# Kernel optimization log

Measured on AMD Instinct MI355X. Metric: run time of the kernel, lower is better.

The kernel has to match this reference:

```python
import jax, jax.numpy as jnp
import numpy as np

L, B, S, D, W = 3, 32, 512, 512, 3
EPS = 1e-6

def setup_inputs() -> dict:
    key = jax.random.key(0)
    ks = jax.random.split(key, 12)
    s = 1.0 / np.sqrt(D)
    def n(k, shape, scale=1.0):
        return jax.random.normal(k, shape, dtype=jnp.float32) * scale
    return {
        'x': n(ks[0], (B, S, D)),
        'fwd_pad': n(ks[1], (L, W, D), s),
        'bwd_pad': n(ks[2], (L, W, D), s),
        'fwd_w': n(ks[3], (L, W + 1)),
        'bwd_w': n(ks[4], (L, W + 1)),
        'fwd_w1': n(ks[5], (L, D, D), s),
        'fwd_b1': jnp.zeros((L, D), jnp.float32),
        'fwd_w2': n(ks[6], (L, D, D), s),
        'fwd_b2': jnp.zeros((L, D), jnp.float32),
        'fwd_g': jnp.ones((L, D), jnp.float32),
        'fwd_beta': jnp.zeros((L, D), jnp.float32),
        'bwd_w1': n(ks[7], (L, D, D), s),
        'bwd_b1': jnp.zeros((L, D), jnp.float32),
        'bwd_w2': n(ks[8], (L, D, D), s),
        'bwd_b2': jnp.zeros((L, D), jnp.float32),
        'bwd_g': jnp.ones((L, D), jnp.float32),
        'bwd_beta': jnp.zeros((L, D), jnp.float32),
    }

def _ln(y, g, b):
    # Annotated-transformer LayerNorm: a2*(x-mean)/(std+eps)+b2, unbiased std
    m = y.mean(-1, keepdims=True)
    sd = jnp.std(y, -1, keepdims=True, ddof=1)
    return g * (y - m) / (sd + EPS) + b

def _ffn(y, w1, b1, w2, b2):
    h = jax.nn.relu(jnp.einsum('bsd,de->bse', y, w1) + b1)
    return jnp.einsum('bse,ef->bsf', h, w2) + b2

def _wsum(padded, w, seq_len, offset):
    # weighted sum over a sliding window of width W+1 (dropout=0, eval mode)
    win = jnp.stack([padded[:, offset + k: offset + k + seq_len] for k in range(W + 1)], 0)
    return jnp.einsum('k,kbsd->bsd', w, win)

def reference(x, fwd_pad, bwd_pad, fwd_w, bwd_w,
              fwd_w1, fwd_b1, fwd_w2, fwd_b2, fwd_g, fwd_beta,
              bwd_w1, bwd_b1, bwd_w2, bwd_b2, bwd_g, bwd_beta):
    bsz, seq_len, _ = x.shape
    xf, xb = x, x
    outs = []
    for i in range(L):
        fp = jnp.broadcast_to(fwd_pad[i], (bsz, W, D))
        bp = jnp.broadcast_to(bwd_pad[i], (bsz, W, D))
        pf = jnp.concatenate([fp, xf, bp], axis=1)  # [B, S+2W, D]
        pb = jnp.concatenate([fp, xb, bp], axis=1)
        yf = _wsum(pf, fwd_w[i], seq_len, 0)       # windows [t, t+W]
        yb = _wsum(pb, bwd_w[i], seq_len, W)       # windows [t+W, t+2W]
        xf = yf + _ffn(_ln(yf, fwd_g[i], fwd_beta[i]), fwd_w1[i], fwd_b1[i], fwd_w2[i], fwd_b2[i])
        xb = yb + _ffn(_ln(yb, bwd_g[i], bwd_beta[i]), bwd_w1[i], bwd_b1[i], bwd_w2[i], bwd_b2[i])
        outs.append(jnp.concatenate([xf, xb], axis=-1))
    return jnp.stack(outs, 0)  # [L, B, S, 2D]
```

## Files before the change

kernel.cpp:

```cpp
#include <hip/hip_runtime.h>

#define S_LEN 512
#define D_DIM 512
#define BATCH 32
#define M_ROWS (BATCH * S_LEN)
#define NLAYER 3

typedef unsigned short ushort_t;
typedef __bf16 bf16_t;
typedef bf16_t bf16x8 __attribute__((ext_vector_type(8)));
typedef unsigned short u16x8 __attribute__((ext_vector_type(8)));
typedef float f32x4 __attribute__((ext_vector_type(4)));

typedef const __attribute__((address_space(1))) unsigned int* gptr_t;
typedef __attribute__((address_space(3))) unsigned int* lptr_t;

__device__ __forceinline__ ushort_t f2bf(float f) {
  unsigned u = __float_as_uint(f);
  unsigned r = (u + 0x7fffu + ((u >> 16) & 1u)) >> 16;
  return (ushort_t)r;
}

__device__ __forceinline__ float4 f4fma(float w, float4 u, float4 a) {
  a.x = fmaf(w, u.x, a.x); a.y = fmaf(w, u.y, a.y);
  a.z = fmaf(w, u.z, a.z); a.w = fmaf(w, u.w, a.w);
  return a;
}

__global__ __launch_bounds__(256)
void wprep_kernel(const float* __restrict__ fw1, const float* __restrict__ fw2,
                  const float* __restrict__ bw1, const float* __restrict__ bw2,
                  ushort_t* __restrict__ wt1, ushort_t* __restrict__ wt2) {
  int z = blockIdx.z;
  int l = z >> 2, m = z & 3;
  const float* bases[4] = {fw1, fw2, bw1, bw2};
  const float* src = bases[m] + (size_t)l * D_DIM * D_DIM;
  int streamIdx = m >> 1;
  int which = m & 1;
  ushort_t* dst = (which ? wt2 : wt1) + ((size_t)streamIdx * NLAYER + l) * D_DIM * D_DIM;

  __shared__ float tile[32][33];
  int n0 = blockIdx.x * 32, k0 = blockIdx.y * 32;
  int tx = threadIdx.x, ty = threadIdx.y;
#pragma unroll
  for (int i = 0; i < 32; i += 8)
    tile[ty + i][tx] = src[(size_t)(k0 + ty + i) * D_DIM + n0 + tx];
  __syncthreads();
#pragma unroll
  for (int i = 0; i < 32; i += 8)
    dst[(size_t)(n0 + ty + i) * D_DIM + k0 + tx] = f2bf(tile[tx][ty + i]);
}

__global__ __launch_bounds__(256, 4)
void conv_ln_kernel(const float* __restrict__ srcF, int strideF,
                    const float* __restrict__ srcB, int strideB,
                    const float* __restrict__ padLo, const float* __restrict__ padHi,
                    const float* __restrict__ wF, const float* __restrict__ wB,
                    const float* __restrict__ gF, const float* __restrict__ beF,
                    const float* __restrict__ gB, const float* __restrict__ beB,
                    ushort_t* __restrict__ yln) {
  int z = blockIdx.y;
  int tid = threadIdx.x;
  int lane = tid & 63;
  int wid = tid >> 6;
  int row0 = (blockIdx.x * 4 + wid) * 4;
  int t0 = row0 & (S_LEN - 1);
  const float* src = z ? srcB : srcF;
  int stride = z ? strideB : strideF;
  const float* wv = z ? wB : wF;
  const float* gv = z ? gB : gF;
  const float* bv = z ? beB : beF;
  int toff = z ? 0 : -3;
  int c0 = lane * 4, c1 = 256 + lane * 4;

  float w0 = wv[0], w1 = wv[1], w2 = wv[2], w3 = wv[3];

  float4 u0[7], u1[7];
#pragma unroll
  for (int q = 0; q < 7; ++q) {
    int tt = t0 + toff + q;
    const float* rp;
    if (tt < 0)            rp = padLo + (size_t)(tt + 3) * D_DIM;
    else if (tt >= S_LEN)  rp = padHi + (size_t)(tt - S_LEN) * D_DIM;
    else                   rp = src + (size_t)(row0 + toff + q) * stride;
    u0[q] = *(const float4*)(rp + c0);
    u1[q] = *(const float4*)(rp + c1);
  }

  float4 g0 = *(const float4*)(gv + c0), g1 = *(const float4*)(gv + c1);
  float4 b0 = *(const float4*)(bv + c0), b1 = *(const float4*)(bv + c1);

  float4 y0[4], y1[4];
#pragma unroll
  for (int j = 0; j < 4; ++j) {
    float4 a = make_float4(0.f, 0.f, 0.f, 0.f);
    a = f4fma(w0, u0[j], a); a = f4fma(w1, u0[j + 1], a);
    a = f4fma(w2, u0[j + 2], a); a = f4fma(w3, u0[j + 3], a);
    y0[j] = a;
    float4 c = make_float4(0.f, 0.f, 0.f, 0.f);
    c = f4fma(w0, u1[j], c); c = f4fma(w1, u1[j + 1], c);
    c = f4fma(w2, u1[j + 2], c); c = f4fma(w3, u1[j + 3], c);
    y1[j] = c;
  }

  float s[4], s2[4];
#pragma unroll
  for (int j = 0; j < 4; ++j) {
    float4 a = y0[j], c = y1[j];
    s[j] = a.x + a.y + a.z + a.w + c.x + c.y + c.z + c.w;
    float t = a.x * a.x;
    t = fmaf(a.y, a.y, t); t = fmaf(a.z, a.z, t); t = fmaf(a.w, a.w, t);
    t = fmaf(c.x, c.x, t); t = fmaf(c.y, c.y, t); t = fmaf(c.z, c.z, t);
    t = fmaf(c.w, c.w, t);
    s2[j] = t;
  }

#pragma unroll
  for (int o = 32; o; o >>= 1) {
#pragma unroll
    for (int j = 0; j < 4; ++j) {
      s[j]  += __shfl_xor(s[j],  o);
      s2[j] += __shfl_xor(s2[j], o);
    }
  }

  size_t base = ((size_t)z * M_ROWS + row0) * D_DIM;
#pragma unroll
  for (int j = 0; j < 4; ++j) {
    float mean = s[j] * (1.0f / 512.0f);
    float qv = fmaf(-512.0f * mean, mean, s2[j]);
    qv = fmaxf(qv, 0.0f);
    float sd = sqrtf(qv * (1.0f / 511.0f));
    float inv = 1.0f / (sd + 1e-6f);
    ushort_t p0[4], p1[4];
    p0[0] = f2bf(g0.x * ((y0[j].x - mean) * inv) + b0.x);
    p0[1] = f2bf(g0.y * ((y0[j].y - mean) * inv) + b0.y);
    p0[2] = f2bf(g0.z * ((y0[j].z - mean) * inv) + b0.z);
    p0[3] = f2bf(g0.w * ((y0[j].w - mean) * inv) + b0.w);
    p1[0] = f2bf(g1.x * ((y1[j].x - mean) * inv) + b1.x);
    p1[1] = f2bf(g1.y * ((y1[j].y - mean) * inv) + b1.y);
    p1[2] = f2bf(g1.z * ((y1[j].z - mean) * inv) + b1.z);
    p1[3] = f2bf(g1.w * ((y1[j].w - mean) * inv) + b1.w);
    *(uint2*)(yln + base + (size_t)j * D_DIM + c0) = *(uint2*)p0;
    *(uint2*)(yln + base + (size_t)j * D_DIM + c1) = *(uint2*)p1;
  }
}

#define PHASE_PRE()                                         \
  __builtin_amdgcn_sched_barrier(0);                        \
  __builtin_amdgcn_s_barrier();                             \
  asm volatile("s_waitcnt lgkmcnt(0)" ::: "memory");        \
  __builtin_amdgcn_sched_barrier(0);                        \
  __builtin_amdgcn_s_setprio(1);

#define PHASE_PRE_NOLGKM()                                  \
  __builtin_amdgcn_sched_barrier(0);                        \
  __builtin_amdgcn_s_barrier();                             \
  __builtin_amdgcn_s_setprio(1);

#define PHASE_POST()                                        \
  __builtin_amdgcn_s_setprio(0);                            \
  __builtin_amdgcn_sched_barrier(0);                        \
  __builtin_amdgcn_s_barrier();

#define GROUP_END_CK4()                                     \
  __builtin_amdgcn_s_setprio(0);                            \
  __builtin_amdgcn_sched_barrier(0);                        \
  asm volatile("s_waitcnt vmcnt(4)" ::: "memory");          \
  __builtin_amdgcn_sched_barrier(0);                        \
  __builtin_amdgcn_s_barrier();

#define GROUP_END_CK0()                                     \
  __builtin_amdgcn_s_setprio(0);                            \
  __builtin_amdgcn_sched_barrier(0);                        \
  asm volatile("s_waitcnt vmcnt(0)" ::: "memory");          \
  __builtin_amdgcn_sched_barrier(0);                        \
  __builtin_amdgcn_s_barrier();

#define READ_A(MH)                                                        \
  _Pragma("unroll")                                                       \
  for (int m_ = 0; m_ < 4; ++m_) {                                        \
    _Pragma("unroll")                                                     \
    for (int kk_ = 0; kk_ < 2; ++kk_) {                                   \
      int row_ = ((MH) * 4 + m_) * 32 + wr16lm;                           \
      int idx_ = (row_ * 64 + kk_ * 32 + lq * 8) ^ ((row_ & 7) * 8);      \
      union { u16x8 u; bf16x8 b; } t_;                                    \
      t_.u = *(const u16x8*)&pa[idx_];                                    \
      aF[kk_][m_] = t_.b;                                                 \
    }                                                                     \
  }

#define READ_B(NH)                                                        \
  _Pragma("unroll")                                                       \
  for (int n_ = 0; n_ < 2; ++n_) {                                        \
    _Pragma("unroll")                                                     \
    for (int kk_ = 0; kk_ < 2; ++kk_) {                                   \
      int row_ = ((NH) * 2 + n_) * 64 + wc16lm;                           \
      int idx_ = (row_ * 64 + kk_ * 32 + lq * 8) ^ ((row_ & 7) * 8);      \
      union { u16x8 u; bf16x8 b; } t_;                                    \
      t_.u = *(const u16x8*)&pb[idx_];                                    \
      bF[NH][kk_][n_] = t_.b;                                             \
    }                                                                     \
  }

#define MFMA16(MH, NH)                                                    \
  _Pragma("unroll")                                                       \
  for (int kk_ = 0; kk_ < 2; ++kk_)                                       \
    _Pragma("unroll")                                                     \
    for (int m_ = 0; m_ < 4; ++m_)                                        \
      _Pragma("unroll")                                                   \
      for (int n_ = 0; n_ < 2; ++n_)                                      \
        acc[(MH) * 4 + m_][(NH) * 2 + n_] =                               \
            __builtin_amdgcn_mfma_f32_16x16x32_bf16(                      \
                aF[kk_][m_], bF[NH][kk_][n_],                             \
                acc[(MH) * 4 + m_][(NH) * 2 + n_], 0, 0, 0);

template <int EPI>
__global__ __launch_bounds__(512, 2)
void gemm256_kernel(const ushort_t* __restrict__ A,
                    const ushort_t* __restrict__ Bt_f, const ushort_t* __restrict__ Bt_b,
                    const float* __restrict__ bias_f, const float* __restrict__ bias_b,
                    ushort_t* __restrict__ Hout,
                    float* __restrict__ Cout,
                    const float* __restrict__ srcF, const float* __restrict__ srcB,
                    int srcStride,
                    const float* __restrict__ padLo, const float* __restrict__ padHi,
                    const float* __restrict__ wF, const float* __restrict__ wB) {
  const int K = 512;
  int bid = blockIdx.x;
  int G = (bid & 7) * 32 + (bid >> 3);
  int z = G >> 7;
  int t2 = G & 127;
  int mblk = t2 >> 1, nblk = t2 & 1;
  int row0 = mblk * 256, n0 = nblk * 256;

  const ushort_t* Ab = A + (size_t)z * M_ROWS * K + (size_t)row0 * K;
  const ushort_t* Bb = (z ? Bt_b : Bt_f) + (size_t)n0 * K;

  __shared__ __attribute__((aligned(16))) ushort_t As[2][256 * 64];
  __shared__ __attribute__((aligned(16))) ushort_t Bs[2][256 * 64];

  int tid = threadIdx.x, lane = tid & 63, wave = tid >> 6;
  int wr = wave >> 2, wc = wave & 3;
  int lm = lane & 15, lq = lane >> 4;
  int wr16lm = wr * 16 + lm;
  int wc16lm = wc * 16 + lm;

  auto STAGE = [&](const ushort_t* src, ushort_t* dstBase, int half, int g) {
#pragma unroll
    for (int u = 0; u < 2; ++u) {
      int ch = u * 512 + tid;
      int r = ch >> 3;
      int cs = ((ch & 7) ^ (r & 7)) * 8;
      __builtin_amdgcn_global_load_lds(
          (gptr_t)(const void*)(src + (size_t)(half * 128 + r) * 512 + g * 64 + cs),
          (lptr_t)(void*)(dstBase + (half * 128 + r) * 64 + (ch & 7) * 8), 16, 0, 0);
    }
  };

  f32x4 acc[8][4] = {};
  bf16x8 aF[2][4];
  bf16x8 bF[2][2][2];

  STAGE(Ab, &As[0][0], 0, 0);
  STAGE(Bb, &Bs[0][0], 0, 0);
  STAGE(Ab, &As[0][0], 1, 0);
  STAGE(Bb, &Bs[0][0], 1, 0);
  STAGE(Ab, &As[1][0], 0, 1);
  STAGE(Bb, &Bs[1][0], 0, 1);
  asm volatile("s_waitcnt vmcnt(4)" ::: "memory");
  __builtin_amdgcn_sched_barrier(0);
  __builtin_amdgcn_s_barrier();

#pragma unroll
  for (int g = 0; g < 8; ++g) {
    const ushort_t* pa = &As[g & 1][0];
    const ushort_t* pb = &Bs[g & 1][0];
    ushort_t* oa = &As[(g & 1) ^ 1][0];
    ushort_t* ob = &Bs[(g & 1) ^ 1][0];
    ushort_t* ca = &As[g & 1][0];
    ushort_t* cb = &Bs[g & 1][0];

    READ_A(0)
    READ_B(0)
    if (g + 1 < 8) STAGE(Ab, oa, 1, g + 1);
    PHASE_PRE()
    MFMA16(0, 0)
    PHASE_POST()

    READ_B(1)
    if (g + 1 < 8) STAGE(Bb, ob, 1, g + 1);
    PHASE_PRE()
    MFMA16(0, 1)
    PHASE_POST()

    READ_A(1)
    if (g + 2 < 8) STAGE(Ab, ca, 0, g + 2);
    PHASE_PRE()
    MFMA16(1, 0)
    PHASE_POST()

    if (g + 2 < 8) STAGE(Bb, cb, 0, g + 2);
    PHASE_PRE_NOLGKM()
    MFMA16(1, 1)
    if (g < 6) {
      GROUP_END_CK4()
    } else if (g == 6) {
      GROUP_END_CK0()
    } else {
      PHASE_POST()
    }
  }

  const float* bias = z ? bias_b : bias_f;
  if (EPI == 1) {
    ushort_t* Hb = Hout + (size_t)z * M_ROWS * 512;
#pragma unroll
    for (int mf = 0; mf < 8; ++mf) {
      int mbase = row0 + (mf * 2 + wr) * 16 + lq * 4;
#pragma unroll
      for (int nf = 0; nf < 4; ++nf) {
        int n = n0 + (nf * 4 + wc) * 16 + lm;
        float bvn = bias[n];
#pragma unroll
        for (int r = 0; r < 4; ++r) {
          float v = fmaxf(acc[mf][nf][r] + bvn, 0.0f);
          Hb[(size_t)(mbase + r) * 512 + n] = f2bf(v);
        }
      }
    }
  } else {
    const float* src = z ? srcB : srcF;
    const float* wv = z ? wB : wF;
    int toff = z ? 0 : -3;
    float w0 = wv[0], w1 = wv[1], w2 = wv[2], w3 = wv[3];
    float* Cb = Cout + (size_t)z * 512;
#pragma unroll
    for (int mf = 0; mf < 8; ++mf) {
      int mbase = row0 + (mf * 2 + wr) * 16 + lq * 4;
      int t0 = mbase & (S_LEN - 1);
      int rb = mbase - t0;
      const float* rp[7];
#pragma unroll
      for (int q = 0; q < 7; ++q) {
        int tt = t0 + toff + q;
        rp[q] = (tt < 0)       ? padLo + (size_t)(tt + 3) * D_DIM
              : (tt >= S_LEN)  ? padHi + (size_t)(tt - S_LEN) * D_DIM
                               : src + (size_t)(rb + tt) * srcStride;
      }
#pragma unroll
      for (int nf = 0; nf < 4; ++nf) {
        int n = n0 + (nf * 4 + wc) * 16 + lm;
        float v[7];
#pragma unroll
        for (int q = 0; q < 7; ++q) v[q] = rp[q][n];
        float bvn = bias[n];
#pragma unroll
        for (int r = 0; r < 4; ++r) {
          float y = w0 * v[r] + w1 * v[r + 1] + w2 * v[r + 2] + w3 * v[r + 3];
          Cb[(size_t)(mbase + r) * 1024 + n] = acc[mf][nf][r] + bvn + y;
        }
      }
    }
  }
}

extern "C" void kernel_launch(void* const* d_in, const int* in_sizes, int n_in,
                              void* d_out, int out_size, void* d_ws, size_t ws_size,
                              hipStream_t stream) {
  const float* x        = (const float*)d_in[0];
  const float* fwd_pad  = (const float*)d_in[1];
  const float* bwd_pad  = (const float*)d_in[2];
  const float* fwd_w    = (const float*)d_in[3];
  const float* bwd_w    = (const float*)d_in[4];
  const float* fwd_w1   = (const float*)d_in[5];
  const float* fwd_b1   = (const float*)d_in[6];
  const float* fwd_w2   = (const float*)d_in[7];
  const float* fwd_b2   = (const float*)d_in[8];
  const float* fwd_g    = (const float*)d_in[9];
  const float* fwd_beta = (const float*)d_in[10];
  const float* bwd_w1   = (const float*)d_in[11];
  const float* bwd_b1   = (const float*)d_in[12];
  const float* bwd_w2   = (const float*)d_in[13];
  const float* bwd_b2   = (const float*)d_in[14];
  const float* bwd_g    = (const float*)d_in[15];
  const float* bwd_beta = (const float*)d_in[16];
  float* out = (float*)d_out;

  const size_t WSZ = (size_t)D_DIM * D_DIM;
  ushort_t* wt1 = (ushort_t*)d_ws;
  ushort_t* wt2 = wt1 + 2 * NLAYER * WSZ;
  ushort_t* yln = wt2 + 2 * NLAYER * WSZ;
  ushort_t* h   = yln + (size_t)2 * M_ROWS * D_DIM;

  wprep_kernel<<<dim3(16, 16, 12), dim3(32, 8), 0, stream>>>(
      fwd_w1, fwd_w2, bwd_w1, bwd_w2, wt1, wt2);

  for (int l = 0; l < NLAYER; ++l) {
    const float *srcF, *srcB;
    int str;
    if (l == 0) {
      srcF = x; srcB = x; str = 512;
    } else {
      srcF = out + (size_t)(l - 1) * M_ROWS * 1024;
      srcB = srcF + 512;
      str = 1024;
    }
    const float* pLo = fwd_pad + (size_t)l * 3 * D_DIM;
    const float* pHi = bwd_pad + (size_t)l * 3 * D_DIM;

    conv_ln_kernel<<<dim3(M_ROWS / 16, 2), 256, 0, stream>>>(
        srcF, str, srcB, str, pLo, pHi,
        fwd_w + l * 4, bwd_w + l * 4,
        fwd_g + l * D_DIM, fwd_beta + l * D_DIM,
        bwd_g + l * D_DIM, bwd_beta + l * D_DIM,
        yln);

    gemm256_kernel<1><<<256, 512, 0, stream>>>(
        yln, wt1 + (size_t)l * WSZ, wt1 + (size_t)(NLAYER + l) * WSZ,
        fwd_b1 + l * D_DIM, bwd_b1 + l * D_DIM,
        h, nullptr,
        nullptr, nullptr, 0, nullptr, nullptr, nullptr, nullptr);

    gemm256_kernel<2><<<256, 512, 0, stream>>>(
        h, wt2 + (size_t)l * WSZ, wt2 + (size_t)(NLAYER + l) * WSZ,
        fwd_b2 + l * D_DIM, bwd_b2 + l * D_DIM,
        nullptr, out + (size_t)l * M_ROWS * 1024,
        srcF, srcB, str, pLo, pHi,
        fwd_w + l * 4, bwd_w + l * 4);
  }
}
```

Baseline: 488.4 us.

## Retile FFN GEMM to 128x512 blocks with K=32 stages

Changes each GEMM block from a 256x256 tile with a K=64 step to a 128-row by full-512-column tile with a K=32 step and 16 pipeline stages. The LDS swizzle, staging pattern, wave-to-fragment mapping and wait-count schedule are rewritten to match. Each block now covers full output rows, so A is read from global memory only once, while B (the whole weight matrix) is re-streamed by every block. LDS per block stays similar, but the pipeline is deeper with more barriers per K step.

```diff
diff --git a/kernel.cpp b/kernel.cpp
--- a/kernel.cpp
+++ b/kernel.cpp
@@ -146,169 +146,134 @@
   }
 }
 
-#define PHASE_PRE()                                         \
-  __builtin_amdgcn_sched_barrier(0);                        \
+#define SB() __builtin_amdgcn_sched_barrier(0)
+
+#define GPHASE_PRE()                                        \
+  SB();                                                     \
   __builtin_amdgcn_s_barrier();                             \
   asm volatile("s_waitcnt lgkmcnt(0)" ::: "memory");        \
-  __builtin_amdgcn_sched_barrier(0);                        \
+  SB();                                                     \
   __builtin_amdgcn_s_setprio(1);
 
-#define PHASE_PRE_NOLGKM()                                  \
-  __builtin_amdgcn_sched_barrier(0);                        \
-  __builtin_amdgcn_s_barrier();                             \
-  __builtin_amdgcn_s_setprio(1);
-
-#define PHASE_POST()                                        \
+#define GPHASE_POST(VM)                                     \
   __builtin_amdgcn_s_setprio(0);                            \
-  __builtin_amdgcn_sched_barrier(0);                        \
+  SB();                                                     \
+  asm volatile("s_waitcnt vmcnt(" #VM ")" ::: "memory");    \
+  SB();                                                     \
   __builtin_amdgcn_s_barrier();
 
-#define GROUP_END_CK4()                                     \
-  __builtin_amdgcn_s_setprio(0);                            \
-  __builtin_amdgcn_sched_barrier(0);                        \
-  asm volatile("s_waitcnt vmcnt(4)" ::: "memory");          \
-  __builtin_amdgcn_sched_barrier(0);                        \
-  __builtin_amdgcn_s_barrier();
-
-#define GROUP_END_CK0()                                     \
-  __builtin_amdgcn_s_setprio(0);                            \
-  __builtin_amdgcn_sched_barrier(0);                        \
-  asm volatile("s_waitcnt vmcnt(0)" ::: "memory");          \
-  __builtin_amdgcn_sched_barrier(0);                        \
-  __builtin_amdgcn_s_barrier();
-
-#define READ_A(MH)                                                        \
+#define READ_AF()                                                         \
   _Pragma("unroll")                                                       \
   for (int m_ = 0; m_ < 4; ++m_) {                                        \
+    int row_ = wr * 64 + m_ * 16 + lm;                                    \
+    int idx_ = row_ * 32 + ((lq ^ ((row_ >> 1) & 3)) * 8);                \
+    union { u16x8 u; bf16x8 b; } t_;                                      \
+    t_.u = *(const u16x8*)&pa[idx_];                                      \
+    aF[m_] = t_.b;                                                        \
+  }
+
+#define READ_BF(PH)                                                       \
+  _Pragma("unroll")                                                       \
+  for (int n_ = 0; n_ < 4; ++n_) {                                        \
+    int row_ = wc * 128 + ((PH) * 4 + n_) * 16 + lm;                      \
+    int idx_ = row_ * 32 + ((lq ^ ((row_ >> 1) & 3)) * 8);                \
+    union { u16x8 u; bf16x8 b; } t_;                                      \
+    t_.u = *(const u16x8*)&pb[idx_];                                      \
+    bF[n_] = t_.b;                                                        \
+  }
+
+#define MFMA_PH(PH)                                                       \
+  _Pragma("unroll")                                                       \
+  for (int m_ = 0; m_ < 4; ++m_)                                          \
     _Pragma("unroll")                                                     \
-    for (int kk_ = 0; kk_ < 2; ++kk_) {                                   \
-      int row_ = ((MH) * 4 + m_) * 32 + wr16lm;                           \
-      int idx_ = (row_ * 64 + kk_ * 32 + lq * 8) ^ ((row_ & 7) * 8);      \
-      union { u16x8 u; bf16x8 b; } t_;                                    \
-      t_.u = *(const u16x8*)&pa[idx_];                                    \
-      aF[kk_][m_] = t_.b;                                                 \
-    }                                                                     \
-  }
-
-#define READ_B(NH)                                                        \
-  _Pragma("unroll")                                                       \
-  for (int n_ = 0; n_ < 2; ++n_) {                                        \
-    _Pragma("unroll")                                                     \
-    for (int kk_ = 0; kk_ < 2; ++kk_) {                                   \
-      int row_ = ((NH) * 2 + n_) * 64 + wc16lm;                           \
-      int idx_ = (row_ * 64 + kk_ * 32 + lq * 8) ^ ((row_ & 7) * 8);      \
-      union { u16x8 u; bf16x8 b; } t_;                                    \
-      t_.u = *(const u16x8*)&pb[idx_];                                    \
-      bF[NH][kk_][n_] = t_.b;                                             \
-    }                                                                     \
-  }
-
-#define MFMA16(MH, NH)                                                    \
-  _Pragma("unroll")                                                       \
-  for (int kk_ = 0; kk_ < 2; ++kk_)                                       \
-    _Pragma("unroll")                                                     \
-    for (int m_ = 0; m_ < 4; ++m_)                                        \
-      _Pragma("unroll")                                                   \
-      for (int n_ = 0; n_ < 2; ++n_)                                      \
-        acc[(MH) * 4 + m_][(NH) * 2 + n_] =                               \
-            __builtin_amdgcn_mfma_f32_16x16x32_bf16(                      \
-                aF[kk_][m_], bF[NH][kk_][n_],                             \
-                acc[(MH) * 4 + m_][(NH) * 2 + n_], 0, 0, 0);
+    for (int n_ = 0; n_ < 4; ++n_)                                        \
+      acc[m_][(PH) * 4 + n_] =                                            \
+          __builtin_amdgcn_mfma_f32_16x16x32_bf16(                        \
+              aF[m_], bF[n_], acc[m_][(PH) * 4 + n_], 0, 0, 0);
 
 template <int EPI>
 __global__ __launch_bounds__(512, 2)
-void gemm256_kernel(const ushort_t* __restrict__ A,
-                    const ushort_t* __restrict__ Bt_f, const ushort_t* __restrict__ Bt_b,
-                    const float* __restrict__ bias_f, const float* __restrict__ bias_b,
-                    ushort_t* __restrict__ Hout,
-                    float* __restrict__ Cout,
-                    const float* __restrict__ srcF, const float* __restrict__ srcB,
-                    int srcStride,
-                    const float* __restrict__ padLo, const float* __restrict__ padHi,
-                    const float* __restrict__ wF, const float* __restrict__ wB) {
+void gemmN_kernel(const ushort_t* __restrict__ A,
+                  const ushort_t* __restrict__ Bt_f, const ushort_t* __restrict__ Bt_b,
+                  const float* __restrict__ bias_f, const float* __restrict__ bias_b,
+                  ushort_t* __restrict__ Hout,
+                  float* __restrict__ Cout,
+                  const float* __restrict__ srcF, const float* __restrict__ srcB,
+                  int srcStride,
+                  const float* __restrict__ padLo, const float* __restrict__ padHi,
+                  const float* __restrict__ wF, const float* __restrict__ wB) {
   const int K = 512;
   int bid = blockIdx.x;
   int G = (bid & 7) * 32 + (bid >> 3);
   int z = G >> 7;
-  int t2 = G & 127;
-  int mblk = t2 >> 1, nblk = t2 & 1;
-  int row0 = mblk * 256, n0 = nblk * 256;
+  int mblk = G & 127;
+  int row0 = mblk * 128;
 
   const ushort_t* Ab = A + (size_t)z * M_ROWS * K + (size_t)row0 * K;
-  const ushort_t* Bb = (z ? Bt_b : Bt_f) + (size_t)n0 * K;
-
-  __shared__ __attribute__((aligned(16))) ushort_t As[2][256 * 64];
-  __shared__ __attribute__((aligned(16))) ushort_t Bs[2][256 * 64];
+  const ushort_t* Bb = z ? Bt_b : Bt_f;
+
+  __shared__ __attribute__((aligned(16))) ushort_t As[2][128 * 32];
+  __shared__ __attribute__((aligned(16))) ushort_t Bs[2][512 * 32];
 
   int tid = threadIdx.x, lane = tid & 63, wave = tid >> 6;
   int wr = wave >> 2, wc = wave & 3;
   int lm = lane & 15, lq = lane >> 4;
-  int wr16lm = wr * 16 + lm;
-  int wc16lm = wc * 16 + lm;
-
-  auto STAGE = [&](const ushort_t* src, ushort_t* dstBase, int half, int g) {
+
+  auto STAGE_A = [&](int g, ushort_t* dst) {
+    int r = tid >> 2, c = tid & 3;
+    int cs = c ^ ((r >> 1) & 3);
+    __builtin_amdgcn_global_load_lds(
+        (gptr_t)(const void*)(Ab + (size_t)r * 512 + g * 32 + cs * 8),
+        (lptr_t)(void*)(dst + tid * 8), 16, 0, 0);
+  };
+  auto STAGE_B = [&](int g, ushort_t* dst, int s) {
 #pragma unroll
     for (int u = 0; u < 2; ++u) {
-      int ch = u * 512 + tid;
-      int r = ch >> 3;
-      int cs = ((ch & 7) ^ (r & 7)) * 8;
+      int i = (u * 512 + tid) >> 2, c = tid & 3;
+      int r = (i & 63) + ((i >> 6) << 7) + s * 64;
+      int cs = c ^ ((r >> 1) & 3);
       __builtin_amdgcn_global_load_lds(
-          (gptr_t)(const void*)(src + (size_t)(half * 128 + r) * 512 + g * 64 + cs),
-          (lptr_t)(void*)(dstBase + (half * 128 + r) * 64 + (ch & 7) * 8), 16, 0, 0);
+          (gptr_t)(const void*)(Bb + (size_t)r * 512 + g * 32 + cs * 8),
+          (lptr_t)(void*)(dst + r * 32 + c * 8), 16, 0, 0);
     }
   };
 
-  f32x4 acc[8][4] = {};
-  bf16x8 aF[2][4];
-  bf16x8 bF[2][2][2];
-
-  STAGE(Ab, &As[0][0], 0, 0);
-  STAGE(Bb, &Bs[0][0], 0, 0);
-  STAGE(Ab, &As[0][0], 1, 0);
-  STAGE(Bb, &Bs[0][0], 1, 0);
-  STAGE(Ab, &As[1][0], 0, 1);
-  STAGE(Bb, &Bs[1][0], 0, 1);
-  asm volatile("s_waitcnt vmcnt(4)" ::: "memory");
-  __builtin_amdgcn_sched_barrier(0);
+  f32x4 acc[4][8] = {};
+  bf16x8 aF[4], bF[4];
+
+  STAGE_A(0, &As[0][0]);
+  STAGE_B(0, &Bs[0][0], 0);
+  STAGE_B(0, &Bs[0][0], 1);
+  STAGE_A(1, &As[1][0]);
+  STAGE_B(1, &Bs[1][0], 0);
+  asm volatile("s_waitcnt vmcnt(3)" ::: "memory");
+  SB();
   __builtin_amdgcn_s_barrier();
 
 #pragma unroll
-  for (int g = 0; g < 8; ++g) {
+  for (int g = 0; g < 16; ++g) {
     const ushort_t* pa = &As[g & 1][0];
     const ushort_t* pb = &Bs[g & 1][0];
-    ushort_t* oa = &As[(g & 1) ^ 1][0];
-    ushort_t* ob = &Bs[(g & 1) ^ 1][0];
-    ushort_t* ca = &As[g & 1][0];
-    ushort_t* cb = &Bs[g & 1][0];
-
-    READ_A(0)
-    READ_B(0)
-    if (g + 1 < 8) STAGE(Ab, oa, 1, g + 1);
-    PHASE_PRE()
-    MFMA16(0, 0)
-    PHASE_POST()
-
-    READ_B(1)
-    if (g + 1 < 8) STAGE(Bb, ob, 1, g + 1);
-    PHASE_PRE()
-    MFMA16(0, 1)
-    PHASE_POST()
-
-    READ_A(1)
-    if (g + 2 < 8) STAGE(Ab, ca, 0, g + 2);
-    PHASE_PRE()
-    MFMA16(1, 0)
-    PHASE_POST()
-
-    if (g + 2 < 8) STAGE(Bb, cb, 0, g + 2);
-    PHASE_PRE_NOLGKM()
-    MFMA16(1, 1)
-    if (g < 6) {
-      GROUP_END_CK4()
-    } else if (g == 6) {
-      GROUP_END_CK0()
-    } else {
-      PHASE_POST()
+    ushort_t* na = &As[(g & 1) ^ 1][0];
+    ushort_t* nb = &Bs[(g & 1) ^ 1][0];
+
+    READ_AF()
+    READ_BF(0)
+    if (g + 1 < 16) STAGE_B(g + 1, nb, 1);
+    GPHASE_PRE()
+    MFMA_PH(0)
+    if (g < 15) { GPHASE_POST(5) } else { GPHASE_POST(0) }
+
+    READ_BF(1)
+    if (g + 2 < 16) { STAGE_A(g + 2, (ushort_t*)pa); STAGE_B(g + 2, (ushort_t*)pb, 0); }
+    GPHASE_PRE()
+    MFMA_PH(1)
+    if (g < 14) { GPHASE_POST(5) }
+    else if (g == 14) { GPHASE_POST(2) }
+    else {
+      __builtin_amdgcn_s_setprio(0);
+      SB();
+      __builtin_amdgcn_s_barrier();
     }
   }
 
@@ -316,11 +281,11 @@
   if (EPI == 1) {
     ushort_t* Hb = Hout + (size_t)z * M_ROWS * 512;
 #pragma unroll
-    for (int mf = 0; mf < 8; ++mf) {
-      int mbase = row0 + (mf * 2 + wr) * 16 + lq * 4;
-#pragma unroll
-      for (int nf = 0; nf < 4; ++nf) {
-        int n = n0 + (nf * 4 + wc) * 16 + lm;
+    for (int mf = 0; mf < 4; ++mf) {
+      int mbase = row0 + wr * 64 + mf * 16 + lq * 4;
+#pragma unroll
+      for (int nf = 0; nf < 8; ++nf) {
+        int n = wc * 128 + nf * 16 + lm;
         float bvn = bias[n];
 #pragma unroll
         for (int r = 0; r < 4; ++r) {
@@ -336,8 +301,8 @@
     float w0 = wv[0], w1 = wv[1], w2 = wv[2], w3 = wv[3];
     float* Cb = Cout + (size_t)z * 512;
 #pragma unroll
-    for (int mf = 0; mf < 8; ++mf) {
-      int mbase = row0 + (mf * 2 + wr) * 16 + lq * 4;
+    for (int mf = 0; mf < 4; ++mf) {
+      int mbase = row0 + wr * 64 + mf * 16 + lq * 4;
       int t0 = mbase & (S_LEN - 1);
       int rb = mbase - t0;
       const float* rp[7];
@@ -349,8 +314,8 @@
                                : src + (size_t)(rb + tt) * srcStride;
       }
 #pragma unroll
-      for (int nf = 0; nf < 4; ++nf) {
-        int n = n0 + (nf * 4 + wc) * 16 + lm;
+      for (int nf = 0; nf < 8; ++nf) {
+        int n = wc * 128 + nf * 16 + lm;
         float v[7];
 #pragma unroll
         for (int q = 0; q < 7; ++q) v[q] = rp[q][n];
@@ -416,13 +381,13 @@
         bwd_g + l * D_DIM, bwd_beta + l * D_DIM,
         yln);
 
-    gemm256_kernel<1><<<256, 512, 0, stream>>>(
+    gemmN_kernel<1><<<256, 512, 0, stream>>>(
         yln, wt1 + (size_t)l * WSZ, wt1 + (size_t)(NLAYER + l) * WSZ,
         fwd_b1 + l * D_DIM, bwd_b1 + l * D_DIM,
         h, nullptr,
         nullptr, nullptr, 0, nullptr, nullptr, nullptr, nullptr);
 
-    gemm256_kernel<2><<<256, 512, 0, stream>>>(
+    gemmN_kernel<2><<<256, 512, 0, stream>>>(
         h, wt2 + (size_t)l * WSZ, wt2 + (size_t)(NLAYER + l) * WSZ,
         fwd_b2 + l * D_DIM, bwd_b2 + l * D_DIM,
         nullptr, out + (size_t)l * M_ROWS * 1024,
```

Result: slower. 529.6 us (+8.4%).
